# Kernel optimization log

Hardware: AMD Instinct MI355X
Metric: run time of the kernel (lower is better)

The kernel has to match this reference:

```python
import jax, jax.numpy as jnp
import numpy as np
import math

EPS = 1e-6
NOISE = 1e-5

def _icnn(x, w0r, b0, w1r, b1, zw, g0r, g1r, ob):
    # x: [..., D]; returns [..., P, D]
    w0 = jax.nn.softplus(w0r) ** 2            # [P, 2D, D]
    w1 = jax.nn.softplus(w1r) ** 2            # [P, D, 2D]
    g0 = jax.nn.sigmoid(g0r)[:, None]          # [P, 1]
    g1 = jax.nn.sigmoid(g1r)[:, None]
    z0 = jax.nn.softplus((jnp.einsum('...d,pkd->...pk', x, w0) + b0) * g0)  # [..., P, 2D]
    xw1 = jnp.einsum('...pk,pdk->...pd', z0, w1) + b1                        # [..., P, D]
    zmap = jnp.einsum('...pk,pkd->...pd', z0, zw)
    z1 = jax.nn.softplus(xw1 * g1 + zmap)
    return z1 + ob

def _convex_gate(x, gw, gb):
    u = jax.nn.softplus(jnp.einsum('...d,od->...o', x, gw) + gb)
    return 1.0 - jnp.exp(-u)  # [..., 1]

def _scalar_hull(x, w0r, b0, w1r, b1, zw, g0r, g1r, ob, gw, gb, key):
    g = _convex_gate(x, gw, gb)
    xg = (x + jax.random.normal(key, x.shape, x.dtype) * NOISE) * g
    r = jnp.sqrt(jnp.mean(xg * xg, axis=-1, keepdims=True) + EPS)
    tau = jnp.exp(0.30343 * r + 0.22159)
    scores = _icnn(xg, w0r, b0, w1r, b1, zw, g0r, g1r, ob).mean(-1)  # [..., P]
    lse = jax.nn.logsumexp(scores * tau, axis=-1, keepdims=True)
    return jnp.squeeze(lse / tau, -1)

def _mixer(q, k, v, mask, qp, kp, whq, whk):
    keys = jax.random.split(jax.random.key(42), 6)
    gate_q = jax.nn.softplus(q)
    q = q * gate_q
    r = jnp.sqrt(jnp.mean(q * q, axis=-1, keepdims=True) + EPS)  # [B,H,S,1]
    tau = jnp.exp(0.30343 * r + 0.22159)
    fq = _scalar_hull(q, *qp, keys[0])  # [B,H,S]
    gk = _scalar_hull(k, *kp, keys[1])
    # creative: perturbed dual evaluations, detached delta
    qn = (jax.random.uniform(keys[2], q.shape, q.dtype) - 0.5) * NOISE
    kn = (jax.random.uniform(keys[3], k.shape, k.dtype) - 0.5) * NOISE
    fq_ = _scalar_hull(q + qn, *qp, keys[4])
    gk_ = _scalar_hull(k + kn, *kp, keys[5])
    fq = fq - 0.1 * jax.lax.stop_gradient(fq_ - fq)
    gk = gk - 0.1 * jax.lax.stop_gradient(gk_ - gk)
    phi_q = jax.nn.softplus(jnp.minimum(jnp.einsum('bhsd,rd->bhsr', q, whq), 20.0))
    phi_k = jax.nn.softplus(jnp.minimum(jnp.einsum('bhsd,rd->bhsr', k, whk), 20.0))
    # LSE_r(log(phi_q+eps) + log(phi_k+eps)) == log((phi_q+eps) @ (phi_k+eps)^T), exactly
    logK = jnp.log(jnp.einsum('bhir,bhjr->bhij', phi_q + EPS, phi_k + EPS))
    scores = fq[..., None] + gk[..., None, :] + logK + jnp.log(jnp.maximum(mask, EPS))
    logits = scores * tau  # tau [B,H,S,1] broadcasts over keys
    log_w = logits - jax.nn.logsumexp(logits, axis=-1, keepdims=True)
    w = jnp.exp(log_w)
    out = jnp.einsum('bhij,bhjd->bhid', w, v)
    a = jax.nn.softmax(w.sum(-3), axis=-1).mean(1)  # [B, S]
    mn = a.min(-1, keepdims=True)
    mx = a.max(-1, keepdims=True)
    a = (a - mn) / (mx - mn + EPS)
    return out, a

def setup_inputs() -> dict:
    B, H, S, D, P, R = 2, 8, 1024, 64, 8, 16
    d1 = 2 * D
    key = jax.random.key(0)
    ks = jax.random.split(key, 32)
    mean0 = math.log(math.sqrt(2.0 / D))
    mean1 = math.log(math.sqrt(2.0 / d1))
    def hull_params(i):
        kk = jax.random.split(ks[i], 6)
        return dict(
            w0=mean0 + 0.2 * jax.random.normal(kk[0], (P, d1, D)),
            b0=jnp.zeros((P, d1)),
            w1=mean1 + 0.2 * jax.random.normal(kk[1], (P, D, d1)),
            b1=jnp.zeros((P, D)),
            zw=jax.random.uniform(kk[2], (P, d1, D), minval=-1.0, maxval=1.0) / math.sqrt(d1 * D) * math.sqrt(6.0),
            g0=jnp.full((P,), -3.0),
            g1=jnp.full((P,), -3.0),
            ob=jnp.zeros((P, D)),
            gw=jax.random.normal(kk[3], (1, D)) / math.sqrt(D),
            gb=jnp.zeros((1,)),
        )
    qp = hull_params(10)
    kp = hull_params(11)
    inp = {
        'q': jax.random.normal(ks[0], (B, H, S, D)),
        'k': jax.random.normal(ks[1], (B, H, S, D)),
        'v': jax.random.normal(ks[2], (B, H, S, D)),
        'mask': jax.random.uniform(ks[3], (B, H, S, S)),
        'whq': jax.random.normal(ks[4], (R, D)) / math.sqrt(D),
        'whk': jax.random.normal(ks[5], (R, D)) / math.sqrt(D),
    }
    for name, p in (('q', qp), ('k', kp)):
        for pn, pv in p.items():
            inp[f'{name}_{pn}'] = pv
    return inp

def reference(q, k, v, mask,
              q_w0, q_b0, q_w1, q_b1, q_zw, q_g0, q_g1, q_ob, q_gw, q_gb,
              k_w0, k_b0, k_w1, k_b1, k_zw, k_g0, k_g1, k_ob, k_gw, k_gb,
              whq, whk):
    qp = (q_w0, q_b0, q_w1, q_b1, q_zw, q_g0, q_g1, q_ob, q_gw, q_gb)
    kp = (k_w0, k_b0, k_w1, k_b1, k_zw, k_g0, k_g1, k_ob, k_gw, k_gb)
    return _mixer(q, k, v, mask, qp, kp, whq, whk)
```

## Files before the change

kernel.cpp:

```cpp
#include <hip/hip_runtime.h>
#include <hip/hip_bf16.h>
#include <math.h>

typedef __hip_bfloat16 bf16;
typedef __attribute__((ext_vector_type(8))) short short8;
typedef __attribute__((ext_vector_type(4))) float f32x4;
#define EPSF 1e-6f

__device__ __forceinline__ float b2f(bf16 v){ return __bfloat162float(v); }
__device__ __forceinline__ bf16  f2b(float v){ return __float2bfloat16(v); }
__device__ __forceinline__ float spf(float x){ return x > 20.f ? x : __logf(1.f + __expf(x)); }
__device__ __forceinline__ float sigf(float x){ return 1.f/(1.f + __expf(-x)); }

__device__ __forceinline__ float wsum(float v){
#pragma unroll
  for (int m = 32; m; m >>= 1) v += __shfl_xor(v, m, 64);
  return v;
}
__device__ __forceinline__ float wmaxr(float v){
#pragma unroll
  for (int m = 32; m; m >>= 1) v = fmaxf(v, __shfl_xor(v, m, 64));
  return v;
}
__device__ __forceinline__ float wminr(float v){
#pragma unroll
  for (int m = 32; m; m >>= 1) v = fminf(v, __shfl_xor(v, m, 64));
  return v;
}
__device__ __forceinline__ void unp(float fv, float& lo, float& hi){
  unsigned u = __float_as_uint(fv);
  lo = __uint_as_float(u << 16);
  hi = __uint_as_float(u & 0xffff0000u);
}

struct PrepArgs {
  const float* w0r[2]; const float* b0[2]; const float* w1r[2]; const float* b1[2];
  const float* zw[2];  const float* g0[2]; const float* g1[2]; const float* ob[2];
  bf16* W0gB[2]; bf16* MtB[2]; float* b0g[2]; float* B1g[2]; float* obm[2];
};

__global__ __launch_bounds__(256) void prep_kernel(PrepArgs a){
  int idx = blockIdx.x*256 + threadIdx.x;
  int s = idx >> 16, r = idx & 65535;
  {
    int p = r >> 13;
    float g0 = sigf(a.g0[s][p]);
    float w  = spf(a.w0r[s][r]);
    a.W0gB[s][r] = f2b(g0 * w * w);
  }
  {
    int pd = r >> 7, kk = r & 127;
    int p = pd >> 6, d = pd & 63;
    float g1 = sigf(a.g1[s][p]);
    float w  = spf(a.w1r[s][r]);
    float z  = a.zw[s][(p<<13) + (kk<<6) + d];
    a.MtB[s][r] = f2b(g1 * w * w + z);
  }
  if (r < 1024) a.b0g[s][r] = sigf(a.g0[s][r>>7]) * a.b0[s][r];
  if (r < 512)  a.B1g[s][r] = sigf(a.g1[s][r>>6]) * a.b1[s][r];
  if (r < 8) {
    float t = 0.f;
    for (int d = 0; d < 64; ++d) t += a.ob[s][r*64 + d];
    a.obm[s][r] = t * (1.f/64.f);
  }
}

__global__ __launch_bounds__(256) void vprep_kernel(const float* __restrict__ v, bf16* __restrict__ vT){
  __shared__ float vL[64][65];
  int bh = blockIdx.x >> 4, jt = blockIdx.x & 15;
  int j0 = jt * 64, t = threadIdx.x;
  for (int i = 0; i < 16; ++i) {
    int idx = t + i*256;
    int jj = idx >> 6, d = idx & 63;
    vL[jj][d] = v[((long)bh*1024 + j0 + jj)*64 + d];
  }
  __syncthreads();
  for (int i = 0; i < 16; ++i) {
    int idx = t + i*256;
    int dd = idx >> 6, js = idx & 63;
    vT[((long)bh*64 + dd)*1024 + j0 + js] = f2b(vL[js][dd]);
  }
}

struct HullArgs {
  const float* x[2]; const float* gw[2]; const float* gb[2]; const float* wh[2];
  const bf16* W0gB[2]; const bf16* MtB[2];
  const float* b0g[2]; const float* B1g[2]; const float* obm[2];
  float* tauOut; float* fOut[2]; float* phiOut[2];
};

__global__ __launch_bounds__(256) void hull_kernel(HullArgs A){
  __shared__ __align__(16) bf16 xgb[16][72];
  __shared__ __align__(16) bf16 z0[16][1032];
  __shared__ float tauh[16];
  __shared__ float scoreb[16][8];
  int bid = blockIdx.x;
  int s = bid >> 10;
  int isQ = (s == 0);
  long row0 = (long)(bid & 1023) * 16;
  const float* x   = A.x[s];
  const float* gw  = A.gw[s];
  const float* wh  = A.wh[s];
  const bf16* W0gB = A.W0gB[s];
  const bf16* MtB  = A.MtB[s];
  const float* b0g = A.b0g[s];
  const float* B1g = A.B1g[s];
  const float* obm = A.obm[s];
  float* fOut   = A.fOut[s];
  float* phiOut = A.phiOut[s];
  int t = threadIdx.x, lane = t & 63, w = t >> 6;
  float gbf = A.gb[s][0];

  for (int rp = 0; rp < 4; ++rp) {
    int r = rp*4 + w;
    long row = row0 + r;
    float xv = x[row*64 + lane];
    float xh = isQ ? xv * spf(xv) : xv;
    float s1 = wsum(xh * gw[lane]);
    float g = 1.f - __expf(-spf(s1 + gbf));
    float xgv = xh * g;
    float msq = wsum(xgv*xgv)*(1.f/64.f) + EPSF;
    float th = __expf(0.30343f*sqrtf(msq) + 0.22159f);
    if (lane == 0) tauh[r] = th;
    if (isQ) {
      float m2 = wsum(xh*xh)*(1.f/64.f) + EPSF;
      if (lane == 0) A.tauOut[row] = __expf(0.30343f*sqrtf(m2) + 0.22159f);
    }
    xgb[r][lane] = f2b(xgv);
    float myphi = 0.f;
#pragma unroll
    for (int jj = 0; jj < 16; ++jj) {
      float pv = wsum(xh * wh[jj*64 + lane]);
      if (lane == jj) myphi = pv;
    }
    if (lane < 16) phiOut[row*16 + lane] = spf(fminf(myphi, 20.f)) + EPSF;
  }
  __syncthreads();

  {
    int g = lane >> 4, cl = lane & 15;
    short8 a0 = *(const short8*)&xgb[cl][g*8];
    short8 a1 = *(const short8*)&xgb[cl][32 + g*8];
    for (int ct = 0; ct < 16; ++ct) {
      int col = w*256 + ct*16 + cl;
      const short8* bp = (const short8*)(W0gB + col*64);
      short8 b0 = bp[g];
      short8 b1 = bp[4 + g];
      f32x4 acc = {0.f, 0.f, 0.f, 0.f};
      acc = __builtin_amdgcn_mfma_f32_16x16x32_bf16(a0, b0, acc, 0, 0, 0);
      acc = __builtin_amdgcn_mfma_f32_16x16x32_bf16(a1, b1, acc, 0, 0, 0);
      float bb = b0g[col];
#pragma unroll
      for (int rg = 0; rg < 4; ++rg)
        z0[g*4 + rg][col] = f2b(spf(acc[rg] + bb));
    }
  }
  __syncthreads();

  {
    int g = lane >> 4, cl = lane & 15;
    for (int pi = 0; pi < 2; ++pi) {
      int p = w + pi*4;
      short8 af[4];
#pragma unroll
      for (int kc = 0; kc < 4; ++kc)
        af[kc] = *(const short8*)&z0[cl][p*128 + kc*32 + g*8];
      float s0 = 0.f, s1 = 0.f, s2 = 0.f, s3 = 0.f;
#pragma unroll
      for (int nt = 0; nt < 4; ++nt) {
        int dcol = nt*16 + cl;
        const short8* mp = (const short8*)(MtB + (p*64 + dcol)*128);
        f32x4 acc = {0.f, 0.f, 0.f, 0.f};
#pragma unroll
        for (int kc = 0; kc < 4; ++kc)
          acc = __builtin_amdgcn_mfma_f32_16x16x32_bf16(af[kc], mp[kc*4 + g], acc, 0, 0, 0);
        float bb = B1g[p*64 + dcol];
        s0 += spf(acc[0] + bb);
        s1 += spf(acc[1] + bb);
        s2 += spf(acc[2] + bb);
        s3 += spf(acc[3] + bb);
      }
#pragma unroll
      for (int m = 1; m < 16; m <<= 1) {
        s0 += __shfl_xor(s0, m, 64);
        s1 += __shfl_xor(s1, m, 64);
        s2 += __shfl_xor(s2, m, 64);
        s3 += __shfl_xor(s3, m, 64);
      }
      if (cl == 0) {
        scoreb[g*4+0][p] = s0 * (1.f/64.f);
        scoreb[g*4+1][p] = s1 * (1.f/64.f);
        scoreb[g*4+2][p] = s2 * (1.f/64.f);
        scoreb[g*4+3][p] = s3 * (1.f/64.f);
      }
    }
  }
  __syncthreads();

  if (t < 16) {
    int r = t;
    float th = tauh[r];
    float li[8]; float m = -1e30f;
#pragma unroll
    for (int p = 0; p < 8; ++p) { li[p] = (scoreb[r][p] + obm[p]) * th; m = fmaxf(m, li[p]); }
    float ssum = 0.f;
#pragma unroll
    for (int p = 0; p < 8; ++p) ssum += __expf(li[p] - m);
    fOut[row0 + r] = (m + __logf(ssum)) / th;
  }
}

__global__ __launch_bounds__(512) void attn3_kernel(
  const float* __restrict__ mask, const bf16* __restrict__ vT,
  const float* __restrict__ phiQ, const float* __restrict__ phiK,
  const float* __restrict__ fqA, const float* __restrict__ gkA, const float* __restrict__ tauA,
  float* __restrict__ aAcc, float* __restrict__ outO)
{
  __shared__ __align__(16) bf16 ebf[16][1032];
  __shared__ __align__(16) float sm[8][1024];
  __shared__ float phq[8][16];
  __shared__ float fqs[8], taus[8], sinvL[8];
  int t = threadIdx.x, lane = t & 63, w = t >> 6;
  int b = blockIdx.x >> 7, it = blockIdx.x & 127;
  int i0 = it * 8;

  {
    float* z = (float*)&ebf[8][0];
    for (int idx = t; idx < 4128; idx += 512) z[idx] = 0.f;
  }

  for (int h = 0; h < 8; ++h) {
    int bh = b*8 + h;
    long pbase = (long)bh * 1024;
    if (t < 128) { int r = t >> 4, c = t & 15;
      phq[r][c] = phiQ[(pbase + i0 + r)*16 + c]; }
    else if (t < 136) { int r = t - 128; fqs[r] = fqA[pbase + i0 + r]; }
    else if (t < 144) { int r = t - 136; taus[r] = tauA[pbase + i0 + r]; }
    __syncthreads();

    float l[16];
    {
      float pq[16];
#pragma unroll
      for (int c = 0; c < 16; ++c) pq[c] = phq[w][c];
      float fq = fqs[w], ta = taus[w];
      const float* pkb = phiK + pbase*16;
      const float* mrow = mask + (pbase + i0 + w)*1024;
      const float* gkb = gkA + pbase;
#pragma unroll 2
      for (int c = 0; c < 16; ++c) {
        int j = c*64 + lane;
        const float4* pk = (const float4*)(pkb + j*16);
        float4 k0 = pk[0], k1 = pk[1], k2 = pk[2], k3 = pk[3];
        float dp = pq[0]*k0.x + pq[1]*k0.y + pq[2]*k0.z + pq[3]*k0.w
                 + pq[4]*k1.x + pq[5]*k1.y + pq[6]*k1.z + pq[7]*k1.w
                 + pq[8]*k2.x + pq[9]*k2.y + pq[10]*k2.z + pq[11]*k2.w
                 + pq[12]*k3.x + pq[13]*k3.y + pq[14]*k3.z + pq[15]*k3.w;
        float mk = fmaxf(mrow[j], EPSF);
        l[c] = (fq + gkb[j] + __logf(dp * mk)) * ta;
      }
    }
    {
      float m = -1e30f;
#pragma unroll
      for (int c = 0; c < 16; ++c) m = fmaxf(m, l[c]);
      m = wmaxr(m);
      float s = 0.f;
#pragma unroll
      for (int c = 0; c < 16; ++c) {
        float e = __expf(l[c] - m);
        s += e;
        ebf[w][c*64 + lane] = f2b(e);
      }
      s = wsum(s);
      if (lane == 0) sinvL[w] = 1.f / s;
    }
    __syncthreads();

    if (w < 4) {
      int g = lane >> 4, cl = lane & 15;
      const short8* bp = (const short8*)(vT + ((long)bh*64 + w*16 + cl)*1024);
      f32x4 cf = {0.f, 0.f, 0.f, 0.f};
      for (int kc = 0; kc < 32; ++kc) {
        short8 aF = *(const short8*)&ebf[cl][kc*32 + g*8];
        short8 bF = bp[kc*4 + g];
        cf = __builtin_amdgcn_mfma_f32_16x16x32_bf16(aF, bF, cf, 0, 0, 0);
      }
      if (g < 2) {
#pragma unroll
        for (int i = 0; i < 4; ++i) {
          int row = g*4 + i;
          outO[(pbase + i0 + row)*64 + w*16 + cl] = cf[i] * sinvL[row];
        }
      }
    } else {
      int r0 = (w-4)*2;
#pragma unroll
      for (int rr = 0; rr < 2; ++rr) {
        int r = r0 + rr;
        float sv = sinvL[r];
#pragma unroll
        for (int ch = 0; ch < 4; ++ch) {
          int jb = ch*256 + lane*4;
          uint2 eb = *(const uint2*)&ebf[r][jb];
          float e0,e1,e2,e3;
          unp(__uint_as_float(eb.x), e0, e1);
          unp(__uint_as_float(eb.y), e2, e3);
          float4 acc;
          if (h == 0) acc = make_float4(0.f,0.f,0.f,0.f);
          else        acc = *(float4*)&sm[r][jb];
          acc.x += sv*e0; acc.y += sv*e1; acc.z += sv*e2; acc.w += sv*e3;
          *(float4*)&sm[r][jb] = acc;
        }
      }
    }
    __syncthreads();
  }

  {
    float l2[16];
    float m = -1e30f;
#pragma unroll
    for (int c = 0; c < 16; ++c) { l2[c] = sm[w][c*64 + lane]; m = fmaxf(m, l2[c]); }
    m = wmaxr(m);
    float s = 0.f;
#pragma unroll
    for (int c = 0; c < 16; ++c) { l2[c] = __expf(l2[c] - m); s += l2[c]; }
    s = wsum(s);
    float sc = 1.f / (s * 1024.f);
#pragma unroll
    for (int c = 0; c < 16; ++c)
      sm[w][c*64 + lane] = l2[c] * sc;
  }
  __syncthreads();
  for (int j = t; j < 1024; j += 512) {
    float ssum = 0.f;
#pragma unroll
    for (int r = 0; r < 8; ++r) ssum += sm[r][j];
    atomicAdd(&aAcc[b*1024 + j], ssum);
  }
}

__global__ __launch_bounds__(1024) void anorm_kernel(const float* __restrict__ aAcc, float* __restrict__ outA){
  int b = blockIdx.x, t = threadIdx.x, lane = t & 63, w = t >> 6;
  float v = aAcc[b*1024 + t];
  __shared__ float rmn[16], rmx[16];
  float mn = wminr(v), mx = wmaxr(v);
  if (lane == 0) { rmn[w] = mn; rmx[w] = mx; }
  __syncthreads();
  mn = rmn[0]; mx = rmx[0];
#pragma unroll
  for (int i = 1; i < 16; ++i) { mn = fminf(mn, rmn[i]); mx = fmaxf(mx, rmx[i]); }
  outA[b*1024 + t] = (v - mn) / (mx - mn + EPSF);
}

extern "C" void kernel_launch(void* const* d_in, const int* in_sizes, int n_in,
                              void* d_out, int out_size, void* d_ws, size_t ws_size,
                              hipStream_t stream)
{
  (void)in_sizes; (void)n_in; (void)out_size; (void)ws_size;
  const float* q    = (const float*)d_in[0];
  const float* k    = (const float*)d_in[1];
  const float* v    = (const float*)d_in[2];
  const float* mask = (const float*)d_in[3];
  const float* whq  = (const float*)d_in[4];
  const float* whk  = (const float*)d_in[5];

  float* ws = (float*)d_ws;
  bf16* w0b_q = (bf16*)(ws);
  bf16* w0b_k = (bf16*)(ws + 32768);
  bf16* mtb_q = (bf16*)(ws + 65536);
  bf16* mtb_k = (bf16*)(ws + 98304);
  float* b0g_q = ws + 131072;
  float* b0g_k = ws + 132096;
  float* B1g_q = ws + 133120;
  float* B1g_k = ws + 133632;
  float* obm_q = ws + 134144;
  float* obm_k = ws + 134160;
  float* tau_q = ws + 134176;
  float* fq_a  = ws + 150560;
  float* gk_a  = ws + 166944;
  float* phi_q = ws + 183328;
  float* phi_k = ws + 445472;
  bf16*  v_T   = (bf16*)(ws + 707616);
  float* a_acc = ws + 1231904;

  hipMemsetAsync(a_acc, 0, 2048*sizeof(float), stream);

  PrepArgs pa;
  for (int s = 0; s < 2; ++s) {
    int o = 6 + 10*s;
    pa.w0r[s] = (const float*)d_in[o+0];
    pa.b0 [s] = (const float*)d_in[o+1];
    pa.w1r[s] = (const float*)d_in[o+2];
    pa.b1 [s] = (const float*)d_in[o+3];
    pa.zw [s] = (const float*)d_in[o+4];
    pa.g0 [s] = (const float*)d_in[o+5];
    pa.g1 [s] = (const float*)d_in[o+6];
    pa.ob [s] = (const float*)d_in[o+7];
  }
  pa.W0gB[0]=w0b_q; pa.W0gB[1]=w0b_k; pa.MtB[0]=mtb_q; pa.MtB[1]=mtb_k;
  pa.b0g[0]=b0g_q; pa.b0g[1]=b0g_k; pa.B1g[0]=B1g_q; pa.B1g[1]=B1g_k;
  pa.obm[0]=obm_q; pa.obm[1]=obm_k;

  prep_kernel<<<512,256,0,stream>>>(pa);
  vprep_kernel<<<256,256,0,stream>>>(v, v_T);

  HullArgs ha;
  ha.x[0] = q; ha.x[1] = k;
  ha.gw[0] = (const float*)d_in[14]; ha.gw[1] = (const float*)d_in[24];
  ha.gb[0] = (const float*)d_in[15]; ha.gb[1] = (const float*)d_in[25];
  ha.wh[0] = whq; ha.wh[1] = whk;
  ha.W0gB[0] = w0b_q; ha.W0gB[1] = w0b_k;
  ha.MtB[0] = mtb_q;  ha.MtB[1] = mtb_k;
  ha.b0g[0] = b0g_q;  ha.b0g[1] = b0g_k;
  ha.B1g[0] = B1g_q;  ha.B1g[1] = B1g_k;
  ha.obm[0] = obm_q;  ha.obm[1] = obm_k;
  ha.tauOut = tau_q;
  ha.fOut[0] = fq_a;  ha.fOut[1] = gk_a;
  ha.phiOut[0] = phi_q; ha.phiOut[1] = phi_k;

  hull_kernel<<<2048,256,0,stream>>>(ha);

  attn3_kernel<<<256,512,0,stream>>>(mask, v_T, phi_q, phi_k, fq_a, gk_a, tau_q,
                                     a_acc, (float*)d_out);
  anorm_kernel<<<2,1024,0,stream>>>(a_acc, (float*)d_out + 1048576);
}
```

Measured before the change: 228.4 us.

## Halve query rows per attention block and split each row across two waves

The attention kernel now handles 4 query rows per block instead of 8 and launches 512 blocks instead of 256. Each row's 1024 keys are split across two waves, and the softmax max and sum are combined through shared memory with extra barriers. The goal is more blocks to fill the GPU's compute units and more latency hiding per row. In exchange, the MFMA tile is half padding, the V tiles are reloaded by twice as many blocks, and there are extra syncs and atomics.

Result: slower. 242.9 us (+6.4%).

```diff
diff --git a/kernel.cpp b/kernel.cpp
--- a/kernel.cpp
+++ b/kernel.cpp
@@ -210,46 +210,48 @@
   }
 }
 
-__global__ __launch_bounds__(512) void attn3_kernel(
+__global__ __launch_bounds__(512) void attn4_kernel(
   const float* __restrict__ mask, const bf16* __restrict__ vT,
   const float* __restrict__ phiQ, const float* __restrict__ phiK,
   const float* __restrict__ fqA, const float* __restrict__ gkA, const float* __restrict__ tauA,
   float* __restrict__ aAcc, float* __restrict__ outO)
 {
   __shared__ __align__(16) bf16 ebf[16][1032];
-  __shared__ __align__(16) float sm[8][1024];
-  __shared__ float phq[8][16];
-  __shared__ float fqs[8], taus[8], sinvL[8];
+  __shared__ __align__(16) float sm[4][1024];
+  __shared__ float phq[4][16];
+  __shared__ float fqs[4], taus[4];
+  __shared__ float wmx[8], wsm2[8];
   int t = threadIdx.x, lane = t & 63, w = t >> 6;
-  int b = blockIdx.x >> 7, it = blockIdx.x & 127;
-  int i0 = it * 8;
-
-  {
-    float* z = (float*)&ebf[8][0];
-    for (int idx = t; idx < 4128; idx += 512) z[idx] = 0.f;
+  int b = blockIdx.x >> 8, it = blockIdx.x & 255;
+  int i0 = it * 4;
+  int r4 = w & 3, jh = w >> 2;
+
+  {
+    float* z = (float*)&ebf[4][0];
+    for (int idx = t; idx < 6192; idx += 512) z[idx] = 0.f;
   }
 
   for (int h = 0; h < 8; ++h) {
     int bh = b*8 + h;
     long pbase = (long)bh * 1024;
-    if (t < 128) { int r = t >> 4, c = t & 15;
+    if (t < 64) { int r = t >> 4, c = t & 15;
       phq[r][c] = phiQ[(pbase + i0 + r)*16 + c]; }
-    else if (t < 136) { int r = t - 128; fqs[r] = fqA[pbase + i0 + r]; }
-    else if (t < 144) { int r = t - 136; taus[r] = tauA[pbase + i0 + r]; }
+    else if (t < 68) { int r = t - 64; fqs[r] = fqA[pbase + i0 + r]; }
+    else if (t < 72) { int r = t - 68; taus[r] = tauA[pbase + i0 + r]; }
     __syncthreads();
 
-    float l[16];
+    float l[8];
     {
       float pq[16];
 #pragma unroll
-      for (int c = 0; c < 16; ++c) pq[c] = phq[w][c];
-      float fq = fqs[w], ta = taus[w];
+      for (int c = 0; c < 16; ++c) pq[c] = phq[r4][c];
+      float fq = fqs[r4], ta = taus[r4];
       const float* pkb = phiK + pbase*16;
-      const float* mrow = mask + (pbase + i0 + w)*1024;
+      const float* mrow = mask + (pbase + i0 + r4)*1024;
       const float* gkb = gkA + pbase;
 #pragma unroll 2
-      for (int c = 0; c < 16; ++c) {
-        int j = c*64 + lane;
+      for (int c = 0; c < 8; ++c) {
+        int j = jh*512 + c*64 + lane;
         const float4* pk = (const float4*)(pkb + j*16);
         float4 k0 = pk[0], k1 = pk[1], k2 = pk[2], k3 = pk[3];
         float dp = pq[0]*k0.x + pq[1]*k0.y + pq[2]*k0.z + pq[3]*k0.w
@@ -263,17 +265,22 @@
     {
       float m = -1e30f;
 #pragma unroll
-      for (int c = 0; c < 16; ++c) m = fmaxf(m, l[c]);
+      for (int c = 0; c < 8; ++c) m = fmaxf(m, l[c]);
       m = wmaxr(m);
+      if (lane == 0) wmx[w] = m;
+    }
+    __syncthreads();
+    {
+      float m = fmaxf(wmx[w], wmx[w ^ 4]);
       float s = 0.f;
 #pragma unroll
-      for (int c = 0; c < 16; ++c) {
+      for (int c = 0; c < 8; ++c) {
         float e = __expf(l[c] - m);
         s += e;
-        ebf[w][c*64 + lane] = f2b(e);
+        ebf[r4][jh*512 + c*64 + lane] = f2b(e);
       }
       s = wsum(s);
-      if (lane == 0) sinvL[w] = 1.f / s;
+      if (lane == 0) wsm2[w] = s;
     }
     __syncthreads();
 
@@ -286,57 +293,61 @@
         short8 bF = bp[kc*4 + g];
         cf = __builtin_amdgcn_mfma_f32_16x16x32_bf16(aF, bF, cf, 0, 0, 0);
       }
-      if (g < 2) {
+      if (g == 0) {
 #pragma unroll
         for (int i = 0; i < 4; ++i) {
-          int row = g*4 + i;
-          outO[(pbase + i0 + row)*64 + w*16 + cl] = cf[i] * sinvL[row];
+          float si = 1.f / (wsm2[i] + wsm2[i + 4]);
+          outO[(pbase + i0 + i)*64 + w*16 + cl] = cf[i] * si;
         }
       }
     } else {
-      int r0 = (w-4)*2;
-#pragma unroll
-      for (int rr = 0; rr < 2; ++rr) {
-        int r = r0 + rr;
-        float sv = sinvL[r];
-#pragma unroll
-        for (int ch = 0; ch < 4; ++ch) {
-          int jb = ch*256 + lane*4;
-          uint2 eb = *(const uint2*)&ebf[r][jb];
-          float e0,e1,e2,e3;
-          unp(__uint_as_float(eb.x), e0, e1);
-          unp(__uint_as_float(eb.y), e2, e3);
-          float4 acc;
-          if (h == 0) acc = make_float4(0.f,0.f,0.f,0.f);
-          else        acc = *(float4*)&sm[r][jb];
-          acc.x += sv*e0; acc.y += sv*e1; acc.z += sv*e2; acc.w += sv*e3;
-          *(float4*)&sm[r][jb] = acc;
-        }
-      }
-    }
-    __syncthreads();
-  }
-
-  {
-    float l2[16];
+      int rv = w - 4;
+      float sv = 1.f / (wsm2[rv] + wsm2[rv + 4]);
+#pragma unroll
+      for (int ch = 0; ch < 4; ++ch) {
+        int jb = ch*256 + lane*4;
+        uint2 eb = *(const uint2*)&ebf[rv][jb];
+        float e0,e1,e2,e3;
+        unp(__uint_as_float(eb.x), e0, e1);
+        unp(__uint_as_float(eb.y), e2, e3);
+        float4 acc;
+        if (h == 0) acc = make_float4(0.f,0.f,0.f,0.f);
+        else        acc = *(float4*)&sm[rv][jb];
+        acc.x += sv*e0; acc.y += sv*e1; acc.z += sv*e2; acc.w += sv*e3;
+        *(float4*)&sm[rv][jb] = acc;
+      }
+    }
+  }
+  __syncthreads();
+
+  float l2[8];
+  {
     float m = -1e30f;
 #pragma unroll
-    for (int c = 0; c < 16; ++c) { l2[c] = sm[w][c*64 + lane]; m = fmaxf(m, l2[c]); }
+    for (int c = 0; c < 8; ++c) { l2[c] = sm[r4][jh*512 + c*64 + lane]; m = fmaxf(m, l2[c]); }
     m = wmaxr(m);
+    if (lane == 0) wmx[w] = m;
+  }
+  __syncthreads();
+  {
+    float m = fmaxf(wmx[w], wmx[w ^ 4]);
     float s = 0.f;
 #pragma unroll
-    for (int c = 0; c < 16; ++c) { l2[c] = __expf(l2[c] - m); s += l2[c]; }
+    for (int c = 0; c < 8; ++c) { l2[c] = __expf(l2[c] - m); s += l2[c]; }
     s = wsum(s);
-    float sc = 1.f / (s * 1024.f);
-#pragma unroll
-    for (int c = 0; c < 16; ++c)
-      sm[w][c*64 + lane] = l2[c] * sc;
+    if (lane == 0) wsm2[w] = s;
+  }
+  __syncthreads();
+  {
+    float s2 = wsm2[r4] + wsm2[r4 + 4];
+    float sc = 1.f / (s2 * 1024.f);
+#pragma unroll
+    for (int c = 0; c < 8; ++c)
+      sm[r4][jh*512 + c*64 + lane] = l2[c] * sc;
   }
   __syncthreads();
   for (int j = t; j < 1024; j += 512) {
-    float ssum = 0.f;
-#pragma unroll
-    for (int r = 0; r < 8; ++r) ssum += sm[r][j];
+    float ssum = sm[0][j] + sm[1][j] + sm[2][j] + sm[3][j];
     atomicAdd(&aAcc[b*1024 + j], ssum);
   }
 }
@@ -422,7 +433,7 @@
 
   hull_kernel<<<2048,256,0,stream>>>(ha);
 
-  attn3_kernel<<<256,512,0,stream>>>(mask, v_T, phi_q, phi_k, fq_a, gk_a, tau_q,
+  attn4_kernel<<<512,512,0,stream>>>(mask, v_T, phi_q, phi_k, fq_a, gk_a, tau_q,
                                      a_acc, (float*)d_out);
   anorm_kernel<<<2,1024,0,stream>>>(a_acc, (float*)d_out + 1048576);
 }
```

## Split attention over head groups with partial softmax buffers and separate reduction kernel

Applied to the files above, without the earlier changes.

Adds a new attention kernel that splits the 8 heads into two groups per block, doubling the grid to 512 blocks. Each block writes its per-row partial head-summed probability maps to workspace instead of finishing the cross-head softmax in place. A second kernel sums the two partials, applies the row softmax and accumulates into the averaged attention buffer. The goal is more parallelism in the attention stage, at the cost of writing and re-reading about 16 MB of partial buffers plus an extra launch. It only runs when the workspace is large enough and otherwise falls back to the old kernel.

New measurement: 233.6 us. 1.02x slower.

```diff
diff --git a/kernel.cpp b/kernel.cpp
--- a/kernel.cpp
+++ b/kernel.cpp
@@ -341,6 +341,156 @@
   }
 }
 
+__global__ __launch_bounds__(512) void attn5_kernel(
+  const float* __restrict__ mask, const bf16* __restrict__ vT,
+  const float* __restrict__ phiQ, const float* __restrict__ phiK,
+  const float* __restrict__ fqA, const float* __restrict__ gkA, const float* __restrict__ tauA,
+  float* __restrict__ smPart0, float* __restrict__ smPart1, float* __restrict__ outO)
+{
+  __shared__ __align__(16) bf16 ebf[16][1032];
+  __shared__ __align__(16) float smp[8][1024];
+  __shared__ float phq[8][16];
+  __shared__ float fqs[8], taus[8], sinvL[8];
+  int t = threadIdx.x, lane = t & 63, w = t >> 6;
+  int b = blockIdx.x >> 8, hg = (blockIdx.x >> 7) & 1, it = blockIdx.x & 127;
+  int i0 = it * 8;
+
+  {
+    float* z = (float*)&ebf[8][0];
+    for (int idx = t; idx < 4128; idx += 512) z[idx] = 0.f;
+  }
+
+  for (int h = 0; h < 4; ++h) {
+    int bh = b*8 + hg*4 + h;
+    long pbase = (long)bh * 1024;
+    if (t < 128) { int r = t >> 4, c = t & 15;
+      phq[r][c] = phiQ[(pbase + i0 + r)*16 + c]; }
+    else if (t < 136) { int r = t - 128; fqs[r] = fqA[pbase + i0 + r]; }
+    else if (t < 144) { int r = t - 136; taus[r] = tauA[pbase + i0 + r]; }
+    __syncthreads();
+
+    float l[16];
+    {
+      float pq[16];
+#pragma unroll
+      for (int c = 0; c < 16; ++c) pq[c] = phq[w][c];
+      float fq = fqs[w], ta = taus[w];
+      const float* pkb = phiK + pbase*16;
+      const float* mrow = mask + (pbase + i0 + w)*1024;
+      const float* gkb = gkA + pbase;
+#pragma unroll 2
+      for (int c = 0; c < 16; ++c) {
+        int j = c*64 + lane;
+        const float4* pk = (const float4*)(pkb + j*16);
+        float4 k0 = pk[0], k1 = pk[1], k2 = pk[2], k3 = pk[3];
+        float dp = pq[0]*k0.x + pq[1]*k0.y + pq[2]*k0.z + pq[3]*k0.w
+                 + pq[4]*k1.x + pq[5]*k1.y + pq[6]*k1.z + pq[7]*k1.w
+                 + pq[8]*k2.x + pq[9]*k2.y + pq[10]*k2.z + pq[11]*k2.w
+                 + pq[12]*k3.x + pq[13]*k3.y + pq[14]*k3.z + pq[15]*k3.w;
+        float mk = fmaxf(mrow[j], EPSF);
+        l[c] = (fq + gkb[j] + __logf(dp * mk)) * ta;
+      }
+    }
+    {
+      float m = -1e30f;
+#pragma unroll
+      for (int c = 0; c < 16; ++c) m = fmaxf(m, l[c]);
+      m = wmaxr(m);
+      float s = 0.f;
+#pragma unroll
+      for (int c = 0; c < 16; ++c) {
+        float e = __expf(l[c] - m);
+        s += e;
+        ebf[w][c*64 + lane] = f2b(e);
+      }
+      s = wsum(s);
+      if (lane == 0) sinvL[w] = 1.f / s;
+    }
+    __syncthreads();
+
+    if (w < 4) {
+      int g = lane >> 4, cl = lane & 15;
+      const short8* bp = (const short8*)(vT + ((long)bh*64 + w*16 + cl)*1024);
+      f32x4 cf = {0.f, 0.f, 0.f, 0.f};
+      for (int kc = 0; kc < 32; ++kc) {
+        short8 aF = *(const short8*)&ebf[cl][kc*32 + g*8];
+        short8 bF = bp[kc*4 + g];
+        cf = __builtin_amdgcn_mfma_f32_16x16x32_bf16(aF, bF, cf, 0, 0, 0);
+      }
+      if (g < 2) {
+#pragma unroll
+        for (int i = 0; i < 4; ++i) {
+          int row = g*4 + i;
+          outO[(pbase + i0 + row)*64 + w*16 + cl] = cf[i] * sinvL[row];
+        }
+      }
+    } else {
+      int r0 = (w-4)*2;
+#pragma unroll
+      for (int rr = 0; rr < 2; ++rr) {
+        int r = r0 + rr;
+        float sv = sinvL[r];
+#pragma unroll
+        for (int ch = 0; ch < 4; ++ch) {
+          int jb = ch*256 + lane*4;
+          uint2 eb = *(const uint2*)&ebf[r][jb];
+          float e0,e1,e2,e3;
+          unp(__uint_as_float(eb.x), e0, e1);
+          unp(__uint_as_float(eb.y), e2, e3);
+          float4 acc;
+          if (h == 0) acc = make_float4(0.f,0.f,0.f,0.f);
+          else        acc = *(float4*)&smp[r][jb];
+          acc.x += sv*e0; acc.y += sv*e1; acc.z += sv*e2; acc.w += sv*e3;
+          *(float4*)&smp[r][jb] = acc;
+        }
+      }
+    }
+    __syncthreads();
+  }
+
+  {
+    float* dst = (hg == 0 ? smPart0 : smPart1) + ((long)b*1024 + i0)*1024;
+    for (int idx = t; idx < 2048; idx += 512) {
+      int r = idx >> 8, j4 = (idx & 255)*4;
+      *(float4*)&dst[(long)r*1024 + j4] = *(const float4*)&smp[r][j4];
+    }
+  }
+}
+
+__global__ __launch_bounds__(256) void smsoft_kernel(
+  const float* __restrict__ p0, const float* __restrict__ p1, float* __restrict__ aAcc)
+{
+  int b = blockIdx.x >> 5, ii = blockIdx.x & 31;
+  int t = threadIdx.x, lane = t & 63, w = t >> 6;
+  __shared__ float redm[4], reds[4];
+  float a0 = 0.f, a1 = 0.f, a2 = 0.f, a3 = 0.f;
+  for (int i = 0; i < 32; ++i) {
+    long row = ((long)b*1024 + ii*32 + i)*1024 + t*4;
+    float4 v0 = *(const float4*)(p0 + row);
+    float4 v1 = *(const float4*)(p1 + row);
+    float4 v = make_float4(v0.x+v1.x, v0.y+v1.y, v0.z+v1.z, v0.w+v1.w);
+    float m = fmaxf(fmaxf(v.x, v.y), fmaxf(v.z, v.w));
+    m = wmaxr(m);
+    if (lane == 0) redm[w] = m;
+    __syncthreads();
+    m = fmaxf(fmaxf(redm[0], redm[1]), fmaxf(redm[2], redm[3]));
+    float4 e;
+    e.x = __expf(v.x - m); e.y = __expf(v.y - m); e.z = __expf(v.z - m); e.w = __expf(v.w - m);
+    float s = e.x + e.y + e.z + e.w;
+    s = wsum(s);
+    if (lane == 0) reds[w] = s;
+    __syncthreads();
+    s = reds[0] + reds[1] + reds[2] + reds[3];
+    float inv = 1.f / (s * 1024.f);
+    a0 += e.x*inv; a1 += e.y*inv; a2 += e.z*inv; a3 += e.w*inv;
+    __syncthreads();
+  }
+  atomicAdd(&aAcc[b*1024 + t*4+0], a0);
+  atomicAdd(&aAcc[b*1024 + t*4+1], a1);
+  atomicAdd(&aAcc[b*1024 + t*4+2], a2);
+  atomicAdd(&aAcc[b*1024 + t*4+3], a3);
+}
+
 __global__ __launch_bounds__(1024) void anorm_kernel(const float* __restrict__ aAcc, float* __restrict__ outA){
   int b = blockIdx.x, t = threadIdx.x, lane = t & 63, w = t >> 6;
   float v = aAcc[b*1024 + t];
@@ -358,7 +508,7 @@
                               void* d_out, int out_size, void* d_ws, size_t ws_size,
                               hipStream_t stream)
 {
-  (void)in_sizes; (void)n_in; (void)out_size; (void)ws_size;
+  (void)in_sizes; (void)n_in; (void)out_size;
   const float* q    = (const float*)d_in[0];
   const float* k    = (const float*)d_in[1];
   const float* v    = (const float*)d_in[2];
@@ -384,6 +534,9 @@
   float* phi_k = ws + 445472;
   bf16*  v_T   = (bf16*)(ws + 707616);
   float* a_acc = ws + 1231904;
+  float* smP0  = ws + 1233952;
+  float* smP1  = ws + 3331104;
+  int useSplit = (ws_size >= (size_t)5428256 * sizeof(float));
 
   hipMemsetAsync(a_acc, 0, 2048*sizeof(float), stream);
 
@@ -422,7 +575,13 @@
 
   hull_kernel<<<2048,256,0,stream>>>(ha);
 
-  attn3_kernel<<<256,512,0,stream>>>(mask, v_T, phi_q, phi_k, fq_a, gk_a, tau_q,
-                                     a_acc, (float*)d_out);
+  if (useSplit) {
+    attn5_kernel<<<512,512,0,stream>>>(mask, v_T, phi_q, phi_k, fq_a, gk_a, tau_q,
+                                       smP0, smP1, (float*)d_out);
+    smsoft_kernel<<<64,256,0,stream>>>(smP0, smP1, a_acc);
+  } else {
+    attn3_kernel<<<256,512,0,stream>>>(mask, v_T, phi_q, phi_k, fq_a, gk_a, tau_q,
+                                       a_acc, (float*)d_out);
+  }
   anorm_kernel<<<2,1024,0,stream>>>(a_acc, (float*)d_out + 1048576);
 }
```

## Split attention heads across two block groups and move head-sum softmax to new kernel

Applied to the files above, without the earlier changes.

The attention kernel now launches twice as many blocks, each covering four of the eight heads, so the GPU has more parallel work. Each head group writes its partial head-summed probability rows to a workspace buffer. A new kernel adds the two partials, applies the row softmax, and atomically accumulates the column sums. This raises occupancy on the 256-CU device at the cost of writing and rereading about 16 MB of partial buffers plus an extra kernel launch.

Result: faster. 220.5 us (-3.5%).

```diff
diff --git a/kernel.cpp b/kernel.cpp
--- a/kernel.cpp
+++ b/kernel.cpp
@@ -210,18 +210,18 @@
   }
 }
 
-__global__ __launch_bounds__(512) void attn3_kernel(
+__global__ __launch_bounds__(512) void attn5_kernel(
   const float* __restrict__ mask, const bf16* __restrict__ vT,
   const float* __restrict__ phiQ, const float* __restrict__ phiK,
   const float* __restrict__ fqA, const float* __restrict__ gkA, const float* __restrict__ tauA,
-  float* __restrict__ aAcc, float* __restrict__ outO)
+  float* __restrict__ smPart0, float* __restrict__ smPart1, float* __restrict__ outO)
 {
   __shared__ __align__(16) bf16 ebf[16][1032];
-  __shared__ __align__(16) float sm[8][1024];
+  __shared__ __align__(16) float smp[8][1024];
   __shared__ float phq[8][16];
   __shared__ float fqs[8], taus[8], sinvL[8];
   int t = threadIdx.x, lane = t & 63, w = t >> 6;
-  int b = blockIdx.x >> 7, it = blockIdx.x & 127;
+  int b = blockIdx.x >> 8, hg = (blockIdx.x >> 7) & 1, it = blockIdx.x & 127;
   int i0 = it * 8;
 
   {
@@ -229,8 +229,8 @@
     for (int idx = t; idx < 4128; idx += 512) z[idx] = 0.f;
   }
 
-  for (int h = 0; h < 8; ++h) {
-    int bh = b*8 + h;
+  for (int h = 0; h < 4; ++h) {
+    int bh = b*8 + hg*4 + h;
     long pbase = (long)bh * 1024;
     if (t < 128) { int r = t >> 4, c = t & 15;
       phq[r][c] = phiQ[(pbase + i0 + r)*16 + c]; }
@@ -308,9 +308,9 @@
           unp(__uint_as_float(eb.y), e2, e3);
           float4 acc;
           if (h == 0) acc = make_float4(0.f,0.f,0.f,0.f);
-          else        acc = *(float4*)&sm[r][jb];
+          else        acc = *(float4*)&smp[r][jb];
           acc.x += sv*e0; acc.y += sv*e1; acc.z += sv*e2; acc.w += sv*e3;
-          *(float4*)&sm[r][jb] = acc;
+          *(float4*)&smp[r][jb] = acc;
         }
       }
     }
@@ -318,27 +318,46 @@
   }
 
   {
-    float l2[16];
-    float m = -1e30f;
-#pragma unroll
-    for (int c = 0; c < 16; ++c) { l2[c] = sm[w][c*64 + lane]; m = fmaxf(m, l2[c]); }
+    float* dst = (hg == 0 ? smPart0 : smPart1) + ((long)b*1024 + i0)*1024;
+    for (int idx = t; idx < 2048; idx += 512) {
+      int r = idx >> 8, j4 = (idx & 255)*4;
+      *(float4*)&dst[(long)r*1024 + j4] = *(const float4*)&smp[r][j4];
+    }
+  }
+}
+
+__global__ __launch_bounds__(256) void smsoft_kernel(
+  const float* __restrict__ p0, const float* __restrict__ p1, float* __restrict__ aAcc)
+{
+  int b = blockIdx.x >> 7, ii = blockIdx.x & 127;
+  int t = threadIdx.x, lane = t & 63, w = t >> 6;
+  __shared__ float redm[4], reds[4];
+  float a0 = 0.f, a1 = 0.f, a2 = 0.f, a3 = 0.f;
+  for (int i = 0; i < 8; ++i) {
+    long row = ((long)b*1024 + ii*8 + i)*1024 + t*4;
+    float4 v0 = *(const float4*)(p0 + row);
+    float4 v1 = *(const float4*)(p1 + row);
+    float4 v = make_float4(v0.x+v1.x, v0.y+v1.y, v0.z+v1.z, v0.w+v1.w);
+    float m = fmaxf(fmaxf(v.x, v.y), fmaxf(v.z, v.w));
     m = wmaxr(m);
-    float s = 0.f;
-#pragma unroll
-    for (int c = 0; c < 16; ++c) { l2[c] = __expf(l2[c] - m); s += l2[c]; }
+    if (lane == 0) redm[w] = m;
+    __syncthreads();
+    m = fmaxf(fmaxf(redm[0], redm[1]), fmaxf(redm[2], redm[3]));
+    float4 e;
+    e.x = __expf(v.x - m); e.y = __expf(v.y - m); e.z = __expf(v.z - m); e.w = __expf(v.w - m);
+    float s = e.x + e.y + e.z + e.w;
     s = wsum(s);
-    float sc = 1.f / (s * 1024.f);
-#pragma unroll
-    for (int c = 0; c < 16; ++c)
-      sm[w][c*64 + lane] = l2[c] * sc;
-  }
-  __syncthreads();
-  for (int j = t; j < 1024; j += 512) {
-    float ssum = 0.f;
-#pragma unroll
-    for (int r = 0; r < 8; ++r) ssum += sm[r][j];
-    atomicAdd(&aAcc[b*1024 + j], ssum);
-  }
+    if (lane == 0) reds[w] = s;
+    __syncthreads();
+    s = reds[0] + reds[1] + reds[2] + reds[3];
+    float inv = 1.f / (s * 1024.f);
+    a0 += e.x*inv; a1 += e.y*inv; a2 += e.z*inv; a3 += e.w*inv;
+    __syncthreads();
+  }
+  atomicAdd(&aAcc[b*1024 + t*4+0], a0);
+  atomicAdd(&aAcc[b*1024 + t*4+1], a1);
+  atomicAdd(&aAcc[b*1024 + t*4+2], a2);
+  atomicAdd(&aAcc[b*1024 + t*4+3], a3);
 }
 
 __global__ __launch_bounds__(1024) void anorm_kernel(const float* __restrict__ aAcc, float* __restrict__ outA){
@@ -384,6 +403,8 @@
   float* phi_k = ws + 445472;
   bf16*  v_T   = (bf16*)(ws + 707616);
   float* a_acc = ws + 1231904;
+  float* smP0  = ws + 1233952;
+  float* smP1  = ws + 3331104;
 
   hipMemsetAsync(a_acc, 0, 2048*sizeof(float), stream);
 
@@ -422,7 +443,8 @@
 
   hull_kernel<<<2048,256,0,stream>>>(ha);
 
-  attn3_kernel<<<256,512,0,stream>>>(mask, v_T, phi_q, phi_k, fq_a, gk_a, tau_q,
-                                     a_acc, (float*)d_out);
+  attn5_kernel<<<512,512,0,stream>>>(mask, v_T, phi_q, phi_k, fq_a, gk_a, tau_q,
+                                     smP0, smP1, (float*)d_out);
+  smsoft_kernel<<<256,256,0,stream>>>(smP0, smP1, a_acc);
   anorm_kernel<<<2,1024,0,stream>>>(a_acc, (float*)d_out + 1048576);
 }
```
